# Optimization experiments

Measured on AMD Instinct MI355X. Metric: run time of the kernel, lower is better.

Reference implementation:

```python
import jax, jax.numpy as jnp
import numpy as np

BLADES = ["", "1", "2", "12"]   # quaternion blades (upstride_type=2)
GEOM = (0, 2, 0)                  # e1^2 = e2^2 = -1


def _square_vector(idx):
    if idx < GEOM[0] + 1:
        return 1
    if idx < GEOM[0] + GEOM[1] + 1:
        return -1
    return 0


def _ga_mul(index_1, index_2):
    # faithful port of GenericLinear._ga_multiply_get_index (compile-time, pure python)
    l1 = [int(c) for c in index_1]
    l2 = [int(c) for c in index_2]
    s, i1, i2, length_l1 = 1, 0, 0, len(l1)
    out_l = []
    while i1 < len(l1) and i2 < len(l2):
        if l1[i1] == l2[i2]:
            if (length_l1 - 1) % 2 != 0:
                s *= -1
            s *= _square_vector(l1[i1])
            length_l1 -= 1
            i1 += 1
            i2 += 1
        elif l1[i1] > l2[i2]:
            if length_l1 % 2 != 0:
                s *= -1
            out_l.append(l2[i2])
            i2 += 1
        else:
            out_l.append(l1[i1])
            length_l1 -= 1
            i1 += 1
    out_l += l1[i1:] + l2[i2:]
    return s, "".join(str(v) for v in out_l)


def _cayley():
    N = len(BLADES)
    tbl = []
    for i in range(N):
        row = []
        for j in range(N):
            s, idx = _ga_mul(BLADES[i], BLADES[j])
            row.append((BLADES.index(idx), s))
        tbl.append(row)
    return tbl


def setup_inputs() -> dict:
    key = jax.random.key(0)
    k1, k2, k3 = jax.random.split(key, 3)
    N, BS, Cin, U = 4, 16384, 256, 256
    x = jax.random.normal(k1, (N * BS, Cin), dtype=jnp.float32)
    W = jax.random.normal(k2, (Cin, N * U), dtype=jnp.float32) * 0.02
    b = jax.random.normal(k3, (N * U,), dtype=jnp.float32) * 0.01
    return {"x": x, "W": W, "b": b}


def reference(x, W, b):
    N = len(BLADES)
    BS = x.shape[0] // N
    U = W.shape[1] // N
    y = x @ W                      # (N*BS, N*U) -- the wrapped Dense (use_bias stripped)
    y = y.reshape(N, BS, N * U)
    y = y.at[0].add(b)             # BiasLayer applied to blade-0 batch chunk only
    cross = y.reshape(N, BS, N, U) # cross[i, :, j, :] = x-blade-i through weight-blade-j
    tbl = _cayley()
    out = [None] * N
    for i in range(N):
        for j in range(N):
            k, s = tbl[i][j]
            t = cross[i, :, j, :] if s == 1 else -cross[i, :, j, :]
            out[k] = t if out[k] is None else out[k] + t
    return jnp.concatenate(out, axis=0)   # (N*BS, U)
```

## Files before the change

kernel.cpp:

```cpp
#include <hip/hip_runtime.h>

using u32 = unsigned int;

typedef __attribute__((ext_vector_type(8))) _Float16 f16x8;
typedef __attribute__((ext_vector_type(4))) float    f32x4;

__global__ __launch_bounds__(256) void build_wcatT(const float* __restrict__ W,
                                                   _Float16* __restrict__ Wt) {
    int t  = blockIdx.x * 256 + threadIdx.x;
    int n  = t >> 10, kk = t & 1023;
    int kb = n >> 8,  u  = n & 255;
    int i  = kk >> 8, c  = kk & 255;
    int j  = i ^ kb;
    float v = W[c * 1024 + j * 256 + u];
    if ((0x3950u >> (i * 4 + kb)) & 1u) v = -v;
    Wt[t] = (_Float16)v;
}

__device__ __forceinline__ void async16(const void* g, void* l) {
    __builtin_amdgcn_global_load_lds((const __attribute__((address_space(1))) u32*)g,
                                     (__attribute__((address_space(3))) u32*)l,
                                     16, 0, 0);
}

#define BARRIER() do { asm volatile("" ::: "memory"); \
                       __builtin_amdgcn_s_barrier(); \
                       asm volatile("" ::: "memory"); } while (0)

#define VMW(n)  asm volatile("s_waitcnt vmcnt(" #n ")" ::: "memory")
#define LGKM0() asm volatile("s_waitcnt lgkmcnt(0)" ::: "memory")
#define SB0()   __builtin_amdgcn_sched_barrier(0)

#define GL16(dst, ptr, off) \
    asm volatile("global_load_dwordx4 %0, %1, off offset:" #off \
                 : "=v"(dst) : "v"(ptr))

#define MFMA(av, bv, c) __builtin_amdgcn_mfma_f32_16x16x32_f16(av, bv, c, 0, 0, 0)

#define PHASE_MFMA(f0, f1, f2, f3) do { \
    __builtin_amdgcn_s_setprio(1); \
    acc[f0][0]=MFMA(a0,b0,acc[f0][0]); acc[f0][1]=MFMA(a0,b1,acc[f0][1]); \
    acc[f0][2]=MFMA(a0,b2,acc[f0][2]); acc[f0][3]=MFMA(a0,b3,acc[f0][3]); \
    acc[f1][0]=MFMA(a1,b0,acc[f1][0]); acc[f1][1]=MFMA(a1,b1,acc[f1][1]); \
    acc[f1][2]=MFMA(a1,b2,acc[f1][2]); acc[f1][3]=MFMA(a1,b3,acc[f1][3]); \
    acc[f2][0]=MFMA(a2,b0,acc[f2][0]); acc[f2][1]=MFMA(a2,b1,acc[f2][1]); \
    acc[f2][2]=MFMA(a2,b2,acc[f2][2]); acc[f2][3]=MFMA(a2,b3,acc[f2][3]); \
    acc[f3][0]=MFMA(a3,b0,acc[f3][0]); acc[f3][1]=MFMA(a3,b1,acc[f3][1]); \
    acc[f3][2]=MFMA(a3,b2,acc[f3][2]); acc[f3][3]=MFMA(a3,b3,acc[f3][3]); \
    __builtin_amdgcn_s_setprio(0); \
    __builtin_amdgcn_sched_barrier(0); \
} while (0)

#define STAGE_B(U, BI) do { \
    const int _b = (BI) * 16384 + 8192; \
    const int _g = (U) * 32; \
    async16(gB0 + _g, lds + _b + tid * 8); \
    async16(gB1 + _g, lds + _b + 4096 + tid * 8); \
} while (0)

#define ISSUE_A(U, d0, d1, d2, d3) do { \
    const float* _p = pA + (size_t)((U) >> 3) * 4194304 + ((U) & 7) * 32; \
    GL16(d0, _p, 0); GL16(d1, _p, 16); \
    const float* _q = _p + 32768; \
    GL16(d2, _q, 0); GL16(d3, _q, 16); \
} while (0)

#define WRITE_A(BI, s0, s1, s2, s3) do { \
    f16x8 h0, h1; \
    h0[0]=(_Float16)(s0)[0]; h0[1]=(_Float16)(s0)[1]; h0[2]=(_Float16)(s0)[2]; h0[3]=(_Float16)(s0)[3]; \
    h0[4]=(_Float16)(s1)[0]; h0[5]=(_Float16)(s1)[1]; h0[6]=(_Float16)(s1)[2]; h0[7]=(_Float16)(s1)[3]; \
    h1[0]=(_Float16)(s2)[0]; h1[1]=(_Float16)(s2)[1]; h1[2]=(_Float16)(s2)[2]; h1[3]=(_Float16)(s2)[3]; \
    h1[4]=(_Float16)(s3)[0]; h1[5]=(_Float16)(s3)[1]; h1[6]=(_Float16)(s3)[2]; h1[7]=(_Float16)(s3)[3]; \
    _Float16* _wp = lds + (BI) * 16384 + aw0; \
    *(f16x8*)(_wp) = h0; \
    *(f16x8*)(_wp + 4096) = h1; \
} while (0)

#define TILE(T, DO_ISSUE, I0,I1,I2,I3, DO_STAGE, DO_WRITE, W0,W1,W2,W3, GATE) do { \
    const _Float16* Ab = lds + ((T) & 3) * 16384; \
    const _Float16* Bb = Ab + 8192; \
    f16x8 a0, a1, a2, a3, b0, b1, b2, b3; \
    a0 = *(const f16x8*)(Ab + aoff);        a1 = *(const f16x8*)(Ab + aoff + 512); \
    a2 = *(const f16x8*)(Ab + aoff + 1024); a3 = *(const f16x8*)(Ab + aoff + 1536); \
    b0 = *(const f16x8*)(Bb + boff);        b1 = *(const f16x8*)(Bb + boff + 512); \
    b2 = *(const f16x8*)(Bb + boff + 1024); b3 = *(const f16x8*)(Bb + boff + 1536); \
    if (DO_ISSUE) { ISSUE_A((T) + 3, I0, I1, I2, I3); } \
    BARRIER(); \
    PHASE_MFMA(0, 1, 2, 3); \
    BARRIER(); \
    a0 = *(const f16x8*)(Ab + aoff + 2048); a1 = *(const f16x8*)(Ab + aoff + 2560); \
    a2 = *(const f16x8*)(Ab + aoff + 3072); a3 = *(const f16x8*)(Ab + aoff + 3584); \
    if (DO_STAGE) { STAGE_B((T) + 2, ((T) + 2) & 3); } \
    GATE; \
    SB0(); \
    if (DO_WRITE) { WRITE_A((((T) + 2) & 3), W0, W1, W2, W3); } \
    BARRIER(); \
    PHASE_MFMA(4, 5, 6, 7); \
    LGKM0(); \
    BARRIER(); \
} while (0)

__global__ __launch_bounds__(512, 2) void ga_gemm(const float* __restrict__ A,
                                                  const _Float16* __restrict__ Bt,
                                                  const float*  __restrict__ bias,
                                                  float* __restrict__ out) {
    __shared__ _Float16 lds[4 * 16384] __attribute__((aligned(16)));

    const int tid  = threadIdx.x;
    const int lane = tid & 63;
    const int wid  = tid >> 6;
    const int wm   = wid >> 2;
    const int wn   = wid & 3;
    const int l15  = lane & 15;
    const int lg   = lane >> 4;

    const int bid = blockIdx.x;
    const int swz = (bid & 7) * 32 + (bid >> 3);
    const int mt  = swz >> 2, nt = swz & 3;
    const int m0  = mt * 256,  n0 = nt * 256;

    const int ar = tid >> 2, ac = tid & 3;
    const float* pA = A + (size_t)(m0 + ar) * 256 + ac * 8;
    const int aw0 = ar * 32 + (ac ^ ((ar >> 1) & 3)) * 8;

    const int s1 = 512 + tid;
    const int r0 = tid >> 2,  r1 = s1 >> 2;
    const int g0 = (tid & 3) ^ ((r0 >> 1) & 3);
    const int g1 = (s1 & 3)  ^ ((r1 >> 1) & 3);
    const _Float16* gB0 = Bt + (size_t)(n0 + r0) * 1024 + g0 * 8;
    const _Float16* gB1 = Bt + (size_t)(n0 + r1) * 1024 + g1 * 8;

    const int sc   = lg ^ ((l15 >> 1) & 3);
    const int aoff = (wm * 128 + l15) * 32 + sc * 8;
    const int boff = (wn * 64  + l15) * 32 + sc * 8;

    f32x4 acc[8][4] = {};
    f32x4 u0, u1, u2, u3, v0, v1, v2, v3;

    ISSUE_A(0, u0, u1, u2, u3);
    ISSUE_A(1, v0, v1, v2, v3);
    STAGE_B(0, 0);
    STAGE_B(1, 1);
    VMW(8);  SB0();
    WRITE_A(0, u0, u1, u2, u3);
    VMW(4);  SB0();
    WRITE_A(1, v0, v1, v2, v3);
    LGKM0();
    ISSUE_A(2, u0, u1, u2, u3);
    VMW(6);
    LGKM0();
    BARRIER();

    for (int t = 0; t < 28; t += 2) {
        TILE(t,     1, v0,v1,v2,v3, 1, 1, u0,u1,u2,u3, VMW(6));
        TILE(t + 1, 1, u0,u1,u2,u3, 1, 1, v0,v1,v2,v3, VMW(6));
    }
    TILE(28, 1, v0,v1,v2,v3, 1, 1, u0,u1,u2,u3, VMW(6));
    TILE(29, 0, u0,u1,u2,u3, 1, 1, v0,v1,v2,v3, VMW(2));
    TILE(30, 0, u0,u1,u2,u3, 0, 0, u0,u1,u2,u3, VMW(0));
    TILE(31, 0, u0,u1,u2,u3, 0, 0, u0,u1,u2,u3, (void)0);

    const size_t outBase = (size_t)nt * 16384 * 256;
    const int ucol = wn * 64 + l15;
    float bv[4];
#pragma unroll
    for (int fn = 0; fn < 4; ++fn) bv[fn] = bias[nt * 256 + ucol + fn * 16];
#pragma unroll
    for (int fm = 0; fm < 8; ++fm) {
        const int m = m0 + wm * 128 + fm * 16 + lg * 4;
#pragma unroll
        for (int r = 0; r < 4; ++r) {
            float* op = out + outBase + (size_t)(m + r) * 256;
#pragma unroll
            for (int fn = 0; fn < 4; ++fn)
                op[ucol + fn * 16] = acc[fm][fn][r] + bv[fn];
        }
    }
}

extern "C" void kernel_launch(void* const* d_in, const int* in_sizes, int n_in,
                              void* d_out, int out_size, void* d_ws, size_t ws_size,
                              hipStream_t stream) {
    (void)in_sizes; (void)n_in; (void)out_size; (void)ws_size;
    const float* x = (const float*)d_in[0];
    const float* W = (const float*)d_in[1];
    const float* b = (const float*)d_in[2];
    float* out = (float*)d_out;

    _Float16* Wt = (_Float16*)d_ws;

    build_wcatT<<<4096, 256, 0, stream>>>(W, Wt);
    ga_gemm<<<256, 512, 0, stream>>>(x, Wt, b, out);
}
```

Baseline: 53.11 us.

## Halve GEMM M-tile to 128 rows and use triple-buffered LDS pipeline

```diff
diff --git a/kernel.cpp b/kernel.cpp
--- a/kernel.cpp
+++ b/kernel.cpp
@@ -37,65 +37,54 @@
 
 #define MFMA(av, bv, c) __builtin_amdgcn_mfma_f32_16x16x32_f16(av, bv, c, 0, 0, 0)
 
-#define PHASE_MFMA(f0, f1, f2, f3) do { \
+#define MM16() do { \
     __builtin_amdgcn_s_setprio(1); \
-    acc[f0][0]=MFMA(a0,b0,acc[f0][0]); acc[f0][1]=MFMA(a0,b1,acc[f0][1]); \
-    acc[f0][2]=MFMA(a0,b2,acc[f0][2]); acc[f0][3]=MFMA(a0,b3,acc[f0][3]); \
-    acc[f1][0]=MFMA(a1,b0,acc[f1][0]); acc[f1][1]=MFMA(a1,b1,acc[f1][1]); \
-    acc[f1][2]=MFMA(a1,b2,acc[f1][2]); acc[f1][3]=MFMA(a1,b3,acc[f1][3]); \
-    acc[f2][0]=MFMA(a2,b0,acc[f2][0]); acc[f2][1]=MFMA(a2,b1,acc[f2][1]); \
-    acc[f2][2]=MFMA(a2,b2,acc[f2][2]); acc[f2][3]=MFMA(a2,b3,acc[f2][3]); \
-    acc[f3][0]=MFMA(a3,b0,acc[f3][0]); acc[f3][1]=MFMA(a3,b1,acc[f3][1]); \
-    acc[f3][2]=MFMA(a3,b2,acc[f3][2]); acc[f3][3]=MFMA(a3,b3,acc[f3][3]); \
+    acc[0][0]=MFMA(a0,b0,acc[0][0]); acc[0][1]=MFMA(a0,b1,acc[0][1]); \
+    acc[0][2]=MFMA(a0,b2,acc[0][2]); acc[0][3]=MFMA(a0,b3,acc[0][3]); \
+    acc[1][0]=MFMA(a1,b0,acc[1][0]); acc[1][1]=MFMA(a1,b1,acc[1][1]); \
+    acc[1][2]=MFMA(a1,b2,acc[1][2]); acc[1][3]=MFMA(a1,b3,acc[1][3]); \
+    acc[2][0]=MFMA(a2,b0,acc[2][0]); acc[2][1]=MFMA(a2,b1,acc[2][1]); \
+    acc[2][2]=MFMA(a2,b2,acc[2][2]); acc[2][3]=MFMA(a2,b3,acc[2][3]); \
+    acc[3][0]=MFMA(a3,b0,acc[3][0]); acc[3][1]=MFMA(a3,b1,acc[3][1]); \
+    acc[3][2]=MFMA(a3,b2,acc[3][2]); acc[3][3]=MFMA(a3,b3,acc[3][3]); \
     __builtin_amdgcn_s_setprio(0); \
     __builtin_amdgcn_sched_barrier(0); \
 } while (0)
 
-#define STAGE_B(U, BI) do { \
-    const int _b = (BI) * 16384 + 8192; \
-    const int _g = (U) * 32; \
-    async16(gB0 + _g, lds + _b + tid * 8); \
-    async16(gB1 + _g, lds + _b + 4096 + tid * 8); \
+#define ISSUE_A(U, d0, d1) do { \
+    const float* _p = pA + (size_t)((U) >> 3) * 4194304 + ((U) & 7) * 32; \
+    GL16(d0, _p, 0); GL16(d1, _p, 16); \
 } while (0)
 
-#define ISSUE_A(U, d0, d1, d2, d3) do { \
-    const float* _p = pA + (size_t)((U) >> 3) * 4194304 + ((U) & 7) * 32; \
-    GL16(d0, _p, 0); GL16(d1, _p, 16); \
-    const float* _q = _p + 32768; \
-    GL16(d2, _q, 0); GL16(d3, _q, 16); \
+#define STAGE_B(U, SB) do { \
+    const int _g = (U) * 32; \
+    _Float16* _d = lds + (SB) * 12288 + 4096 + tid * 8; \
+    async16(gB0 + _g, _d); \
+    async16(gB0 + 131072 + _g, _d + 4096); \
 } while (0)
 
-#define WRITE_A(BI, s0, s1, s2, s3) do { \
-    f16x8 h0, h1; \
-    h0[0]=(_Float16)(s0)[0]; h0[1]=(_Float16)(s0)[1]; h0[2]=(_Float16)(s0)[2]; h0[3]=(_Float16)(s0)[3]; \
-    h0[4]=(_Float16)(s1)[0]; h0[5]=(_Float16)(s1)[1]; h0[6]=(_Float16)(s1)[2]; h0[7]=(_Float16)(s1)[3]; \
-    h1[0]=(_Float16)(s2)[0]; h1[1]=(_Float16)(s2)[1]; h1[2]=(_Float16)(s2)[2]; h1[3]=(_Float16)(s2)[3]; \
-    h1[4]=(_Float16)(s3)[0]; h1[5]=(_Float16)(s3)[1]; h1[6]=(_Float16)(s3)[2]; h1[7]=(_Float16)(s3)[3]; \
-    _Float16* _wp = lds + (BI) * 16384 + aw0; \
-    *(f16x8*)(_wp) = h0; \
-    *(f16x8*)(_wp + 4096) = h1; \
+#define WRITE_A(SB, s0, s1) do { \
+    f16x8 h; \
+    h[0]=(_Float16)(s0)[0]; h[1]=(_Float16)(s0)[1]; \
+    h[2]=(_Float16)(s0)[2]; h[3]=(_Float16)(s0)[3]; \
+    h[4]=(_Float16)(s1)[0]; h[5]=(_Float16)(s1)[1]; \
+    h[6]=(_Float16)(s1)[2]; h[7]=(_Float16)(s1)[3]; \
+    *(f16x8*)(lds + (SB) * 12288 + aw0) = h; \
 } while (0)
 
-#define TILE(T, DO_ISSUE, I0,I1,I2,I3, DO_STAGE, DO_WRITE, W0,W1,W2,W3, GATE) do { \
-    const _Float16* Ab = lds + ((T) & 3) * 16384; \
-    const _Float16* Bb = Ab + 8192; \
+#define TILE(T, BUF, SBUF, DO_ISSUE, I0, I1, DO_STAGE, DO_WRITE, W0, W1, GATE, GATE2) do { \
+    const _Float16* Ab = lds + (BUF) * 12288; \
     f16x8 a0, a1, a2, a3, b0, b1, b2, b3; \
     a0 = *(const f16x8*)(Ab + aoff);        a1 = *(const f16x8*)(Ab + aoff + 512); \
     a2 = *(const f16x8*)(Ab + aoff + 1024); a3 = *(const f16x8*)(Ab + aoff + 1536); \
-    b0 = *(const f16x8*)(Bb + boff);        b1 = *(const f16x8*)(Bb + boff + 512); \
-    b2 = *(const f16x8*)(Bb + boff + 1024); b3 = *(const f16x8*)(Bb + boff + 1536); \
-    if (DO_ISSUE) { ISSUE_A((T) + 3, I0, I1, I2, I3); } \
-    BARRIER(); \
-    PHASE_MFMA(0, 1, 2, 3); \
-    BARRIER(); \
-    a0 = *(const f16x8*)(Ab + aoff + 2048); a1 = *(const f16x8*)(Ab + aoff + 2560); \
-    a2 = *(const f16x8*)(Ab + aoff + 3072); a3 = *(const f16x8*)(Ab + aoff + 3584); \
-    if (DO_STAGE) { STAGE_B((T) + 2, ((T) + 2) & 3); } \
-    GATE; \
-    SB0(); \
-    if (DO_WRITE) { WRITE_A((((T) + 2) & 3), W0, W1, W2, W3); } \
-    BARRIER(); \
-    PHASE_MFMA(4, 5, 6, 7); \
+    b0 = *(const f16x8*)(Ab + boff);        b1 = *(const f16x8*)(Ab + boff + 512); \
+    b2 = *(const f16x8*)(Ab + boff + 1024); b3 = *(const f16x8*)(Ab + boff + 1536); \
+    if (DO_ISSUE) { ISSUE_A((T) + 3, I0, I1); } \
+    if (DO_STAGE) { STAGE_B((T) + 2, SBUF); } \
+    MM16(); \
+    GATE; SB0(); \
+    if (DO_WRITE) { WRITE_A(SBUF, W0, W1); } \
+    GATE2; \
     LGKM0(); \
     BARRIER(); \
 } while (0)
@@ -104,7 +93,7 @@
                                                   const _Float16* __restrict__ Bt,
                                                   const float*  __restrict__ bias,
                                                   float* __restrict__ out) {
-    __shared__ _Float16 lds[4 * 16384] __attribute__((aligned(16)));
+    __shared__ _Float16 lds[3 * 12288] __attribute__((aligned(16)));
 
     const int tid  = threadIdx.x;
     const int lane = tid & 63;
@@ -115,50 +104,55 @@
     const int lg   = lane >> 4;
 
     const int bid = blockIdx.x;
-    const int swz = (bid & 7) * 32 + (bid >> 3);
+    const int swz = (bid & 7) * 64 + (bid >> 3);
     const int mt  = swz >> 2, nt = swz & 3;
-    const int m0  = mt * 256,  n0 = nt * 256;
+    const int m0  = mt * 128,  n0 = nt * 256;
 
     const int ar = tid >> 2, ac = tid & 3;
     const float* pA = A + (size_t)(m0 + ar) * 256 + ac * 8;
     const int aw0 = ar * 32 + (ac ^ ((ar >> 1) & 3)) * 8;
 
-    const int s1 = 512 + tid;
-    const int r0 = tid >> 2,  r1 = s1 >> 2;
+    const int r0 = tid >> 2;
     const int g0 = (tid & 3) ^ ((r0 >> 1) & 3);
-    const int g1 = (s1 & 3)  ^ ((r1 >> 1) & 3);
     const _Float16* gB0 = Bt + (size_t)(n0 + r0) * 1024 + g0 * 8;
-    const _Float16* gB1 = Bt + (size_t)(n0 + r1) * 1024 + g1 * 8;
 
     const int sc   = lg ^ ((l15 >> 1) & 3);
-    const int aoff = (wm * 128 + l15) * 32 + sc * 8;
-    const int boff = (wn * 64  + l15) * 32 + sc * 8;
+    const int aoff = (wm * 64 + l15) * 32 + sc * 8;
+    const int boff = 4096 + (wn * 64 + l15) * 32 + sc * 8;
 
-    f32x4 acc[8][4] = {};
-    f32x4 u0, u1, u2, u3, v0, v1, v2, v3;
+    f32x4 acc[4][4] = {};
+    f32x4 u0, u1, v0, v1;
 
-    ISSUE_A(0, u0, u1, u2, u3);
-    ISSUE_A(1, v0, v1, v2, v3);
+    ISSUE_A(0, u0, u1);
+    ISSUE_A(1, v0, v1);
     STAGE_B(0, 0);
     STAGE_B(1, 1);
-    VMW(8);  SB0();
-    WRITE_A(0, u0, u1, u2, u3);
+    VMW(6);  SB0();
+    WRITE_A(0, u0, u1);
     VMW(4);  SB0();
-    WRITE_A(1, v0, v1, v2, v3);
+    WRITE_A(1, v0, v1);
     LGKM0();
-    ISSUE_A(2, u0, u1, u2, u3);
-    VMW(6);
+    ISSUE_A(2, u0, u1);
+    VMW(4);
     LGKM0();
     BARRIER();
 
-    for (int t = 0; t < 28; t += 2) {
-        TILE(t,     1, v0,v1,v2,v3, 1, 1, u0,u1,u2,u3, VMW(6));
-        TILE(t + 1, 1, u0,u1,u2,u3, 1, 1, v0,v1,v2,v3, VMW(6));
+    for (int t = 0; t < 24; t += 6) {
+        TILE(t + 0, 0, 2, 1, v0, v1, 1, 1, u0, u1, VMW(4), (void)0);
+        TILE(t + 1, 1, 0, 1, u0, u1, 1, 1, v0, v1, VMW(4), (void)0);
+        TILE(t + 2, 2, 1, 1, v0, v1, 1, 1, u0, u1, VMW(4), (void)0);
+        TILE(t + 3, 0, 2, 1, u0, u1, 1, 1, v0, v1, VMW(4), (void)0);
+        TILE(t + 4, 1, 0, 1, v0, v1, 1, 1, u0, u1, VMW(4), (void)0);
+        TILE(t + 5, 2, 1, 1, u0, u1, 1, 1, v0, v1, VMW(4), (void)0);
     }
-    TILE(28, 1, v0,v1,v2,v3, 1, 1, u0,u1,u2,u3, VMW(6));
-    TILE(29, 0, u0,u1,u2,u3, 1, 1, v0,v1,v2,v3, VMW(2));
-    TILE(30, 0, u0,u1,u2,u3, 0, 0, u0,u1,u2,u3, VMW(0));
-    TILE(31, 0, u0,u1,u2,u3, 0, 0, u0,u1,u2,u3, (void)0);
+    TILE(24, 0, 2, 1, v0, v1, 1, 1, u0, u1, VMW(4), (void)0);
+    TILE(25, 1, 0, 1, u0, u1, 1, 1, v0, v1, VMW(4), (void)0);
+    TILE(26, 2, 1, 1, v0, v1, 1, 1, u0, u1, VMW(4), (void)0);
+    TILE(27, 0, 2, 1, u0, u1, 1, 1, v0, v1, VMW(4), (void)0);
+    TILE(28, 1, 0, 1, v0, v1, 1, 1, u0, u1, VMW(4), (void)0);
+    TILE(29, 2, 1, 0, u0, u1, 1, 1, v0, v1, VMW(4), VMW(2));
+    TILE(30, 0, 0, 0, u0, u1, 0, 0, u0, u1, VMW(0), (void)0);
+    TILE(31, 1, 0, 0, u0, u1, 0, 0, u0, u1, (void)0, (void)0);
 
     const size_t outBase = (size_t)nt * 16384 * 256;
     const int ucol = wn * 64 + l15;
@@ -166,14 +160,14 @@
 #pragma unroll
     for (int fn = 0; fn < 4; ++fn) bv[fn] = bias[nt * 256 + ucol + fn * 16];
 #pragma unroll
-    for (int fm = 0; fm < 8; ++fm) {
-        const int m = m0 + wm * 128 + fm * 16 + lg * 4;
+    for (int fm = 0; fm < 4; ++fm) {
+        const int m = m0 + wm * 64 + fm * 16 + lg * 4;
 #pragma unroll
-        for (int r = 0; r < 4; ++r) {
-            float* op = out + outBase + (size_t)(m + r) * 256;
+        for (int rr = 0; rr < 4; ++rr) {
+            float* op = out + outBase + (size_t)(m + rr) * 256;
 #pragma unroll
             for (int fn = 0; fn < 4; ++fn)
-                op[ucol + fn * 16] = acc[fm][fn][r] + bv[fn];
+                op[ucol + fn * 16] = acc[fm][fn][rr] + bv[fn];
         }
     }
 }
@@ -190,5 +184,5 @@
     _Float16* Wt = (_Float16*)d_ws;
 
     build_wcatT<<<4096, 256, 0, stream>>>(W, Wt);
-    ga_gemm<<<256, 512, 0, stream>>>(x, Wt, b, out);
+    ga_gemm<<<512, 512, 0, stream>>>(x, Wt, b, out);
 }
```

New measurement: 58.83 us. +10.8%, slower.
